# Optimization experiments

Measured on AMD Instinct MI355X. Metric: run time of the kernel, lower is better.

Reference implementation:

```python
import jax, jax.numpy as jnp
import numpy as np

B, S = 2, 2048          # 2 prompt sequences of 2048 tokens (packed: T = B*S)
H, KV, D, G = 32, 8, 128, 128   # heads, kv heads, head_dim, quant group size
THETA = 1e6


def _dequant(w_int, scales, g=G):
    # w_int: [O, I] int4 values in [-8, 7]; scales: [O, I//g] per-group fp scales
    return w_int.astype(jnp.float32) * jnp.repeat(scales, g, axis=1)


def _rope_neox(x, pos):
    # x: [B, S, h, D]; pos: [B, S]; neox style rotates (first half, second half)
    half = D // 2
    inv_freq = 1.0 / (THETA ** (jnp.arange(half, dtype=jnp.float32) / half))
    ang = pos[:, :, None] * inv_freq[None, None, :]          # [B, S, half]
    cos = jnp.cos(ang)[:, :, None, :]
    sin = jnp.sin(ang)[:, :, None, :]
    x1, x2 = x[..., :half], x[..., half:]
    return jnp.concatenate([x1 * cos - x2 * sin, x2 * cos + x1 * sin], axis=-1)


def setup_inputs() -> dict:
    key = jax.random.key(0)
    k1, k2, k3, k4, k5, k6 = jax.random.split(key, 6)
    T, HID = B * S, H * D
    q_hidden = jax.random.randint(k1, (T, HID), -127, 128, dtype=jnp.int32)  # int8 acts
    q_scale = jax.random.uniform(k2, (T,), dtype=jnp.float32) * 0.01 + 1e-4  # per-token scale
    q_sum = jnp.sum(q_hidden, axis=-1).astype(jnp.float32)                   # per-token int8 sum
    OUT_QKV = (H + 2 * KV) * D
    w_qkv = jax.random.randint(k3, (OUT_QKV, HID), -8, 8, dtype=jnp.int32)   # int4 weights
    s_qkv = jax.random.uniform(k4, (OUT_QKV, HID // G), dtype=jnp.float32) * 0.01 + 1e-4
    w_o = jax.random.randint(k5, (HID, HID), -8, 8, dtype=jnp.int32)
    s_o = jax.random.uniform(k6, (HID, HID // G), dtype=jnp.float32) * 0.01 + 1e-4
    return {"q_hidden": q_hidden, "q_scale": q_scale, "q_sum": q_sum,
            "w_qkv": w_qkv, "s_qkv": s_qkv, "w_o": w_o, "s_o": s_o}


def reference(q_hidden, q_scale, q_sum, w_qkv, s_qkv, w_o, s_o):
    T = q_hidden.shape[0]
    # W4A8 qkv_proj with dynamic per-token input scale (symmetric int4 -> sum unused)
    x = q_hidden.astype(jnp.float32) * q_scale[:, None]          # dequant activations
    qkv = x @ _dequant(w_qkv, s_qkv).T                            # [T, (H+2KV)*D]
    q_sz, kv_sz = H * D, KV * D
    q = qkv[:, :q_sz].reshape(B, S, H, D)
    k = qkv[:, q_sz:q_sz + kv_sz].reshape(B, S, KV, D)
    v = qkv[:, q_sz + kv_sz:].reshape(B, S, KV, D)
    # fused bias(none)+RoPE (neox, full head_dim)
    pos = jnp.broadcast_to(jnp.arange(S, dtype=jnp.float32), (B, S))
    q = _rope_neox(q, pos)
    k = _rope_neox(k, pos)
    # varlen causal flash attention (GQA: 4 q-heads per kv head)
    qg = q.reshape(B, S, KV, H // KV, D)
    scores = jnp.einsum('bsghd,btgd->bghst', qg, k) * (D ** -0.5)
    causal = jnp.tril(jnp.ones((S, S), dtype=bool))
    scores = jnp.where(causal[None, None, None], scores, -jnp.inf)
    p = jax.nn.softmax(scores, axis=-1)
    attn = jnp.einsum('bghst,btgd->bsghd', p, v).reshape(T, H * D)
    # invoke_quant_fuse_sum: per-token symmetric int8 requant of attn output
    amax = jnp.maximum(jnp.max(jnp.abs(attn), axis=-1, keepdims=True), 1e-6)
    a_scale = amax / 127.0
    attn_q = jnp.clip(jnp.round(attn / a_scale), -127.0, 127.0)
    # W4A8 o_proj
    out = (attn_q * a_scale) @ _dequant(w_o, s_o).T               # [T, H*D]
    return out
```

## Files before the change

### kernel.cpp

```cpp
#include <hip/hip_runtime.h>
#include <math.h>

#define B_ 2
#define S_ 2048
#define H_ 32
#define KV_ 8
#define D_ 128
#define T_ 4096
#define HID_ 4096
#define OQKV_ 6144

typedef __attribute__((ext_vector_type(4))) float f32x4;
typedef __attribute__((ext_vector_type(4))) int i32x4;
typedef __attribute__((ext_vector_type(8))) __bf16 bf16x8;
typedef __attribute__((ext_vector_type(8))) unsigned short u16x8;
typedef unsigned short u16;
typedef signed char s8;

__device__ __forceinline__ u16 f2b(float f) {
  unsigned x = __float_as_uint(f);
  return (u16)((x + 0x7FFFu + ((x >> 16) & 1u)) >> 16);
}
__device__ __forceinline__ float b2f(u16 u) {
  return __uint_as_float(((unsigned)u) << 16);
}

__device__ __forceinline__ void async16(const void* g, void* l) {
  __builtin_amdgcn_global_load_lds((__attribute__((address_space(1))) void*)g,
                                   (__attribute__((address_space(3))) void*)l,
                                   16, 0, 0);
}

__device__ __forceinline__ bf16x8 ld8(const u16* p) { return *(const bf16x8*)p; }

__device__ __forceinline__ f32x4 mfma16x16(bf16x8 a, bf16x8 b, f32x4 c) {
  return __builtin_amdgcn_mfma_f32_16x16x32_bf16(a, b, c, 0, 0, 0);
}

__device__ __forceinline__ bf16x8 ones8() {
  union { u16x8 u; bf16x8 b; } c;
  c.u = u16x8{0x3F80, 0x3F80, 0x3F80, 0x3F80, 0x3F80, 0x3F80, 0x3F80, 0x3F80};
  return c.b;
}

__global__ __launch_bounds__(256) void pack_i8(const int* __restrict__ w,
                                               s8* __restrict__ out) {
  size_t base = ((size_t)blockIdx.x * 256 + threadIdx.x) * 4;
  int4 v = *(const int4*)(w + base);
  unsigned r = (unsigned)(v.x & 255) | ((unsigned)(v.y & 255) << 8) |
               ((unsigned)(v.z & 255) << 16) | ((unsigned)v.w << 24);
  *(unsigned*)(out + base) = r;
}

__global__ __launch_bounds__(256) void rope_kernel(u16* __restrict__ qkv) {
  int idx = blockIdx.x * 256 + threadIdx.x;
  int t = idx / 2560;
  int r = idx - t * 2560;
  int head = r >> 6;
  int d = r & 63;
  int col = (head < 32) ? (head * 128 + d) : (4096 + (head - 32) * 128 + d);
  size_t base = (size_t)t * 6144 + col;
  float x1 = b2f(qkv[base]);
  float x2 = b2f(qkv[base + 64]);
  float e = (float)d * 0.015625f;
  float freq = exp2f(e * -19.931568569324174f);
  float ang = (float)(t & 2047) * freq;
  float sn, cs;
  sincosf(ang, &sn, &cs);
  qkv[base] = f2b(x1 * cs - x2 * sn);
  qkv[base + 64] = f2b(x2 * cs + x1 * sn);
}

__global__ __launch_bounds__(256) void vt_transpose(const u16* __restrict__ qkv,
                                                    u16* __restrict__ vt) {
  __shared__ u16 tile[64][65];
  const int s0 = blockIdx.x * 64, d0 = blockIdx.y * 64;
  const int bk = blockIdx.z, b = bk >> 3, kv = bk & 7;
  const int tid = threadIdx.x;
  const int rr = tid >> 3, cc = tid & 7;
#pragma unroll
  for (int it = 0; it < 2; it++) {
    int r = it * 32 + rr;
    u16x8 v = *(const u16x8*)(qkv + (size_t)(b * 2048 + s0 + r) * 6144 + 5120 +
                              kv * 128 + d0 + cc * 8);
#pragma unroll
    for (int k = 0; k < 8; k++) tile[r][cc * 8 + k] = v[k];
  }
  __syncthreads();
#pragma unroll
  for (int it = 0; it < 2; it++) {
    int d = it * 32 + rr;
    u16x8 o;
#pragma unroll
    for (int k = 0; k < 8; k++) o[k] = tile[cc * 8 + k][d];
    *(u16x8*)(vt + (size_t)(bk * 128 + d0 + d) * 2048 + s0 + cc * 8) = o;
  }
}

__device__ __forceinline__ void store_out(float* p, float v) { *p = v; }
__device__ __forceinline__ void store_out(u16* p, float v) { *p = f2b(v); }

template <typename OutT>
__global__ __launch_bounds__(256, 4) void gemm_i8(const s8* __restrict__ A,
                                                  const s8* __restrict__ Bw,
                                                  const float* __restrict__ sB,
                                                  const float* __restrict__ rowscale,
                                                  OutT* __restrict__ C,
                                                  int M, int N, int K) {
  __shared__ __align__(16) s8 As[128 * 128];
  __shared__ __align__(16) s8 Bs[64 * 128];
  __shared__ float Ss[64][33];
  const int tid = threadIdx.x;
  const int lane = tid & 63;
  const int wv = tid >> 6;
  const int m0 = blockIdx.y * 128, n0 = blockIdx.x * 64;
  const int g = lane >> 4, c15 = lane & 15;
  const int KG = K >> 7;

  for (int i = tid; i < 64 * 32; i += 256)
    Ss[i >> 5][i & 31] = sB[(size_t)n0 * 32 + i];

  f32x4 acc[2][4] = {};

  const int srow = lane >> 2;
  const int pch = lane & 3;
  const int scol = (((pch - (srow >> 1)) & 3)) * 16;
  const s8* Ag0 = A + (size_t)(m0 + (2 * wv) * 16 + srow) * K + scol;
  const s8* Ag1 = A + (size_t)(m0 + (2 * wv + 1) * 16 + srow) * K + scol;
  const s8* Bg = Bw + (size_t)(n0 + wv * 16 + srow) * K + scol;
  s8* Al0 = As + (2 * wv) * 1024 + lane * 16;
  s8* Al1 = As + (2 * wv + 1) * 1024 + lane * 16;
  s8* Bl = Bs + wv * 1024 + lane * 16;

  const int aoff = (wv * 32 + c15) * 64 + ((g + (c15 >> 1)) & 3) * 16;
  const int boff = c15 * 64 + ((g + (c15 >> 1)) & 3) * 16;

  for (int grp = 0; grp < KG; ++grp) {
    const int kb = grp << 7;
    __syncthreads();
    async16(Ag0 + kb, Al0);
    async16(Ag1 + kb, Al1);
    async16(Bg + kb, Bl);
    async16(Ag0 + kb + 64, Al0 + 8192);
    async16(Ag1 + kb + 64, Al1 + 8192);
    async16(Bg + kb + 64, Bl + 4096);
    __syncthreads();

    i32x4 iacc[2][4];
#pragma unroll
    for (int sub = 0; sub < 2; sub++) {
      i32x4 af[2], bf[4];
#pragma unroll
      for (int i = 0; i < 2; i++)
        af[i] = *(const i32x4*)(As + sub * 8192 + aoff + i * 1024);
#pragma unroll
      for (int j = 0; j < 4; j++)
        bf[j] = *(const i32x4*)(Bs + sub * 4096 + boff + j * 1024);
#pragma unroll
      for (int i = 0; i < 2; i++)
#pragma unroll
        for (int j = 0; j < 4; j++)
          iacc[i][j] = __builtin_amdgcn_mfma_i32_16x16x64_i8(
              af[i], bf[j], sub ? iacc[i][j] : (i32x4){0, 0, 0, 0}, 0, 0, 0);
    }
#pragma unroll
    for (int j = 0; j < 4; j++) {
      const float sc = Ss[j * 16 + c15][grp];
#pragma unroll
      for (int i = 0; i < 2; i++)
#pragma unroll
        for (int r = 0; r < 4; r++)
          acc[i][j][r] += sc * (float)iacc[i][j][r];
    }
  }

#pragma unroll
  for (int i = 0; i < 2; i++) {
#pragma unroll
    for (int r = 0; r < 4; r++) {
      int m = m0 + wv * 32 + i * 16 + g * 4 + r;
      float scm = rowscale[m];
#pragma unroll
      for (int j = 0; j < 4; j++) {
        int n = n0 + j * 16 + c15;
        store_out(C + (size_t)m * N + n, acc[i][j][r] * scm);
      }
    }
  }
}


struct AttnState {
  f32x4 acc[2][9];
  float mrun[2][4];
};

template <bool FULL>
__device__ __forceinline__ void qk_phase(int j0, int q0w, const u16* Ksp,
                                         const bf16x8 qf[2][4],
                                         f32x4 (&sc)[2][4], int g, int c15) {
  const int qmax = q0w + 31;
#pragma unroll
  for (int nt = 0; nt < 4; nt++) {
    if (FULL || (j0 + nt * 16 <= qmax)) {
      bf16x8 kf[4];
#pragma unroll
      for (int c = 0; c < 4; c++)
        kf[c] = ld8(Ksp + (nt * 16 + c15) * 128 +
                    (((g + 4 * c) ^ (c15 & 7)) * 8));
      f32x4 s0 = {0.f, 0.f, 0.f, 0.f}, s1 = {0.f, 0.f, 0.f, 0.f};
#pragma unroll
      for (int c = 0; c < 4; c++) {
        s0 = mfma16x16(qf[0][c], kf[c], s0);
        s1 = mfma16x16(qf[1][c], kf[c], s1);
      }
      if (FULL) {
#pragma unroll
        for (int r = 0; r < 4; r++) {
          sc[0][nt][r] = s0[r] * 0.08838834764831845f;
          sc[1][nt][r] = s1[r] * 0.08838834764831845f;
        }
      } else {
        const int key = j0 + nt * 16 + c15;
#pragma unroll
        for (int r = 0; r < 4; r++) {
          sc[0][nt][r] =
              (key <= q0w + g * 4 + r) ? s0[r] * 0.08838834764831845f : -INFINITY;
          sc[1][nt][r] =
              (key <= q0w + 16 + g * 4 + r) ? s1[r] * 0.08838834764831845f : -INFINITY;
        }
      }
    }
  }
}

template <bool FULL>
__device__ __forceinline__ void smax_pv(int j0, int q0w, const u16* Vsp,
                                        u16* pw0, u16* pw1, f32x4 (&sc)[2][4],
                                        AttnState& st, int g, int c15,
                                        const bf16x8 vones) {
  const int qmax = q0w + 31;
#pragma unroll
  for (int m = 0; m < 2; m++) {
    u16* pw = m ? pw1 : pw0;
    float alpha[4];
#pragma unroll
    for (int r = 0; r < 4; r++) {
      float rm = -INFINITY;
#pragma unroll
      for (int nt = 0; nt < 4; nt++)
        if (FULL || (j0 + nt * 16 <= qmax)) rm = fmaxf(rm, sc[m][nt][r]);
      rm = fmaxf(rm, __shfl_xor(rm, 1));
      rm = fmaxf(rm, __shfl_xor(rm, 2));
      rm = fmaxf(rm, __shfl_xor(rm, 4));
      rm = fmaxf(rm, __shfl_xor(rm, 8));
      float mnew = fmaxf(st.mrun[m][r], rm);
      alpha[r] = __expf(st.mrun[m][r] - mnew);
      st.mrun[m][r] = mnew;
#pragma unroll
      for (int nt = 0; nt < 4; nt++) {
        float pv = (FULL || (j0 + nt * 16 <= qmax))
                       ? __expf(sc[m][nt][r] - mnew) : 0.0f;
        pw[(g * 4 + r) * 72 + nt * 16 + c15] = f2b(pv);
      }
    }
#pragma unroll
    for (int dt = 0; dt < 9; dt++)
#pragma unroll
      for (int r = 0; r < 4; r++) st.acc[m][dt][r] *= alpha[r];
  }
#pragma unroll
  for (int kc = 0; kc < 2; kc++) {
    bf16x8 pf0 = ld8(pw0 + c15 * 72 + kc * 32 + g * 8);
    bf16x8 pf1 = ld8(pw1 + c15 * 72 + kc * 32 + g * 8);
#pragma unroll
    for (int dt = 0; dt < 8; dt++) {
      bf16x8 vf = ld8(Vsp + (dt * 16 + c15) * 64 +
                      (((g + 4 * kc) ^ (c15 & 7)) * 8));
      st.acc[0][dt] = mfma16x16(pf0, vf, st.acc[0][dt]);
      st.acc[1][dt] = mfma16x16(pf1, vf, st.acc[1][dt]);
    }
    st.acc[0][8] = mfma16x16(pf0, vones, st.acc[0][8]);
    st.acc[1][8] = mfma16x16(pf1, vones, st.acc[1][8]);
  }
}

__global__ __launch_bounds__(256, 2) void attn_kernel(const u16* __restrict__ qkvb,
                                                      const u16* __restrict__ vtb,
                                                      float* __restrict__ out) {
  __shared__ __align__(16) u16 Ks[64 * 128];
  __shared__ __align__(16) u16 Vs[2][128 * 64];
  __shared__ __align__(16) u16 Ps[4][2][16 * 72];
  const int tid = threadIdx.x, lane = tid & 63, wv = tid >> 6;
  const int g = lane >> 4, c15 = lane & 15;
  const int h = blockIdx.x, b = blockIdx.y, qb = 15 - (int)blockIdx.z;
  const int kvh = h >> 2;
  const int Q0 = qb * 128;
  const int q0w = Q0 + wv * 32;
  const int nsteps = 2 * qb + 2;
  const bf16x8 vones = ones8();
  u16* pw0 = &Ps[wv][0][0];
  u16* pw1 = &Ps[wv][1][0];

  const int keyl = lane >> 4, kch = lane & 15;
  const int dll = lane >> 3, vch = lane & 7;
  const u16* Kg = qkvb + (size_t)(b * 2048) * 6144 + 4096 + kvh * 128;
  const u16* Vg = vtb + (size_t)((b * 8 + kvh) * 128) * 2048;

  auto stageK = [&](int j0) {
#pragma unroll
    for (int i = 0; i < 4; i++) {
      const int key = wv * 16 + i * 4 + keyl;
      async16(Kg + (size_t)(j0 + key) * 6144 + ((kch ^ (key & 7)) * 8),
              (u16*)Ks + (wv * 16 + i * 4) * 128 + lane * 8);
    }
  };
  auto stageV = [&](int j0, int vb) {
#pragma unroll
    for (int i = 0; i < 4; i++) {
      const int d = wv * 32 + i * 8 + dll;
      async16(Vg + (size_t)d * 2048 + j0 + ((vch ^ (d & 7)) * 8),
              (u16*)&Vs[vb][0] + (wv * 32 + i * 8) * 64 + lane * 8);
    }
  };

  bf16x8 qf[2][4];
#pragma unroll
  for (int m = 0; m < 2; m++) {
    const u16* qp =
        qkvb + (size_t)(b * 2048 + q0w + m * 16 + c15) * 6144 + h * 128 + g * 8;
#pragma unroll
    for (int c = 0; c < 4; c++) qf[m][c] = ld8(qp + c * 32);
  }

  AttnState st;
#pragma unroll
  for (int m = 0; m < 2; m++) {
#pragma unroll
    for (int dt = 0; dt < 9; dt++) st.acc[m][dt] = f32x4{0.f, 0.f, 0.f, 0.f};
#pragma unroll
    for (int r = 0; r < 4; r++) st.mrun[m][r] = -INFINITY;
  }

  stageK(0);
  stageV(0, 0);

  for (int jt = 0; jt < nsteps; ++jt) {
    const int j0 = jt * 64;
    __syncthreads();
    const int mode = (j0 + 64 <= q0w) ? 0 : ((j0 <= q0w + 31) ? 1 : 2);
    f32x4 sc[2][4];
    if (mode == 0) qk_phase<true>(j0, q0w, (const u16*)Ks, qf, sc, g, c15);
    else if (mode == 1) qk_phase<false>(j0, q0w, (const u16*)Ks, qf, sc, g, c15);
    __syncthreads();
    if (jt + 1 < nsteps) {
      stageK(j0 + 64);
      stageV(j0 + 64, (jt + 1) & 1);
    }
    const u16* Vsp = (const u16*)&Vs[jt & 1][0];
    if (mode == 0) smax_pv<true>(j0, q0w, Vsp, pw0, pw1, sc, st, g, c15, vones);
    else if (mode == 1) smax_pv<false>(j0, q0w, Vsp, pw0, pw1, sc, st, g, c15, vones);
  }

#pragma unroll
  for (int m = 0; m < 2; m++)
#pragma unroll
    for (int r = 0; r < 4; r++) {
      const int row = q0w + m * 16 + g * 4 + r;
      float inv = 1.0f / st.acc[m][8][r];
      float* op = out + (size_t)(b * 2048 + row) * 4096 + h * 128;
#pragma unroll
      for (int dt = 0; dt < 8; dt++) op[dt * 16 + c15] = st.acc[m][dt][r] * inv;
    }
}

__global__ __launch_bounds__(256) void quant_kernel(const float* __restrict__ attn,
                                                    s8* __restrict__ aq,
                                                    float* __restrict__ ascale) {
  const int t = blockIdx.x, tid = threadIdx.x;
  const float* row = attn + (size_t)t * 4096;
  f32x4 v[4];
  float am = 0.f;
#pragma unroll
  for (int i = 0; i < 4; i++) {
    v[i] = *(const f32x4*)(row + tid * 16 + i * 4);
#pragma unroll
    for (int r = 0; r < 4; r++) am = fmaxf(am, fabsf(v[i][r]));
  }
#pragma unroll
  for (int m = 1; m <= 32; m <<= 1) am = fmaxf(am, __shfl_xor(am, m));
  __shared__ float red[4];
  if ((tid & 63) == 0) red[tid >> 6] = am;
  __syncthreads();
  am = fmaxf(fmaxf(red[0], red[1]), fmaxf(red[2], red[3]));
  float asc = fmaxf(am, 1e-6f) / 127.0f;
  if (tid == 0) ascale[t] = asc;
  int w[4];
#pragma unroll
  for (int i = 0; i < 4; i++) {
    int bytes[4];
#pragma unroll
    for (int r = 0; r < 4; r++) {
      float q = rintf(v[i][r] / asc);
      q = fminf(127.0f, fmaxf(-127.0f, q));
      bytes[r] = ((int)q) & 255;
    }
    w[i] = bytes[0] | (bytes[1] << 8) | (bytes[2] << 16) | (bytes[3] << 24);
  }
  *(int4*)(aq + (size_t)t * 4096 + tid * 16) = int4{w[0], w[1], w[2], w[3]};
}

extern "C" void kernel_launch(void* const* d_in, const int* in_sizes, int n_in,
                              void* d_out, int out_size, void* d_ws, size_t ws_size,
                              hipStream_t stream) {
  const int* q_hidden = (const int*)d_in[0];
  const float* q_scale = (const float*)d_in[1];
  const int* w_qkv = (const int*)d_in[3];
  const float* s_qkv = (const float*)d_in[4];
  const int* w_o = (const int*)d_in[5];
  const float* s_o = (const float*)d_in[6];
  float* out = (float*)d_out;

  char* ws = (char*)d_ws;
  const size_t MB = 1024 * 1024;
  s8* WB = (s8*)(ws);
  u16* QKVB = (u16*)(ws + 48 * MB);
  u16* VTB = (u16*)(ws);
  s8* ATTNQ = (s8*)(ws + 8 * MB);
  float* ASC = (float*)(ws + 25 * MB);
  s8* WOB = (s8*)(ws + 48 * MB);
  s8* XB = (s8*)d_out;

  pack_i8<<<16384, 256, 0, stream>>>(q_hidden, XB);
  pack_i8<<<24576, 256, 0, stream>>>(w_qkv, WB);
  gemm_i8<u16><<<dim3(96, 32), 256, 0, stream>>>(XB, WB, s_qkv, q_scale, QKVB,
                                                 T_, OQKV_, HID_);
  rope_kernel<<<40960, 256, 0, stream>>>(QKVB);
  vt_transpose<<<dim3(32, 2, 16), 256, 0, stream>>>(QKVB, VTB);
  attn_kernel<<<dim3(32, 2, 16), 256, 0, stream>>>(QKVB, VTB, out);
  quant_kernel<<<4096, 256, 0, stream>>>(out, ATTNQ, ASC);
  pack_i8<<<16384, 256, 0, stream>>>(w_o, WOB);
  gemm_i8<float><<<dim3(64, 32), 256, 0, stream>>>(ATTNQ, WOB, s_o, ASC, out,
                                                   T_, HID_, HID_);
}
```

Baseline: 665.1 us.

## Double-buffer int8 GEMM K-tiles with async LDS loads and manual waitcnt

The W4A8 int8 GEMM used to load a full 128-wide K slab and sync twice per group, so global loads and MFMA never overlapped. It now keeps two 64-wide LDS buffers and issues the next half-tile's global_load_lds while the current one is consumed. Raw s_barrier and s_waitcnt vmcnt replace __syncthreads, and the loop is software-pipelined across the two halves. Shared memory use stays the same. Correctness now depends on the hand-written vmcnt counts matching the compiler's ordering of memory operations.

Result: slower. 719.1 us (+8.1%).

```diff
diff --git a/kernel.cpp b/kernel.cpp
--- a/kernel.cpp
+++ b/kernel.cpp
@@ -42,6 +42,9 @@
   c.u = u16x8{0x3F80, 0x3F80, 0x3F80, 0x3F80, 0x3F80, 0x3F80, 0x3F80, 0x3F80};
   return c.b;
 }
+
+#define SBAR() asm volatile("s_barrier" ::: "memory")
+#define WAITV(n) asm volatile("s_waitcnt vmcnt(" #n ")" ::: "memory")
 
 __global__ __launch_bounds__(256) void pack_i8(const int* __restrict__ w,
                                                s8* __restrict__ out) {
@@ -107,8 +110,8 @@
                                                   const float* __restrict__ rowscale,
                                                   OutT* __restrict__ C,
                                                   int M, int N, int K) {
-  __shared__ __align__(16) s8 As[128 * 128];
-  __shared__ __align__(16) s8 Bs[64 * 128];
+  __shared__ __align__(16) s8 As[2][128 * 64];
+  __shared__ __align__(16) s8 Bs[2][64 * 64];
   __shared__ float Ss[64][33];
   const int tid = threadIdx.x;
   const int lane = tid & 63;
@@ -116,6 +119,7 @@
   const int m0 = blockIdx.y * 128, n0 = blockIdx.x * 64;
   const int g = lane >> 4, c15 = lane & 15;
   const int KG = K >> 7;
+  const int NT = K >> 6;
 
   for (int i = tid; i < 64 * 32; i += 256)
     Ss[i >> 5][i & 31] = sB[(size_t)n0 * 32 + i];
@@ -128,40 +132,77 @@
   const s8* Ag0 = A + (size_t)(m0 + (2 * wv) * 16 + srow) * K + scol;
   const s8* Ag1 = A + (size_t)(m0 + (2 * wv + 1) * 16 + srow) * K + scol;
   const s8* Bg = Bw + (size_t)(n0 + wv * 16 + srow) * K + scol;
-  s8* Al0 = As + (2 * wv) * 1024 + lane * 16;
-  s8* Al1 = As + (2 * wv + 1) * 1024 + lane * 16;
-  s8* Bl = Bs + wv * 1024 + lane * 16;
+  const int la0 = (2 * wv) * 1024 + lane * 16;
+  const int la1 = (2 * wv + 1) * 1024 + lane * 16;
+  const int lb = wv * 1024 + lane * 16;
 
   const int aoff = (wv * 32 + c15) * 64 + ((g + (c15 >> 1)) & 3) * 16;
   const int boff = c15 * 64 + ((g + (c15 >> 1)) & 3) * 16;
 
+  async16(Ag0, &As[0][0] + la0);
+  async16(Ag1, &As[0][0] + la1);
+  async16(Bg, &Bs[0][0] + lb);
+  async16(Ag0 + 64, &As[1][0] + la0);
+  async16(Ag1 + 64, &As[1][0] + la1);
+  async16(Bg + 64, &Bs[1][0] + lb);
+  asm volatile("s_waitcnt vmcnt(3) lgkmcnt(0)" ::: "memory");
+  SBAR();
+
   for (int grp = 0; grp < KG; ++grp) {
-    const int kb = grp << 7;
-    __syncthreads();
-    async16(Ag0 + kb, Al0);
-    async16(Ag1 + kb, Al1);
-    async16(Bg + kb, Bl);
-    async16(Ag0 + kb + 64, Al0 + 8192);
-    async16(Ag1 + kb + 64, Al1 + 8192);
-    async16(Bg + kb + 64, Bl + 4096);
-    __syncthreads();
-
     i32x4 iacc[2][4];
-#pragma unroll
-    for (int sub = 0; sub < 2; sub++) {
+    {
       i32x4 af[2], bf[4];
 #pragma unroll
       for (int i = 0; i < 2; i++)
-        af[i] = *(const i32x4*)(As + sub * 8192 + aoff + i * 1024);
+        af[i] = *(const i32x4*)(&As[0][0] + aoff + i * 1024);
 #pragma unroll
       for (int j = 0; j < 4; j++)
-        bf[j] = *(const i32x4*)(Bs + sub * 4096 + boff + j * 1024);
+        bf[j] = *(const i32x4*)(&Bs[0][0] + boff + j * 1024);
 #pragma unroll
       for (int i = 0; i < 2; i++)
 #pragma unroll
         for (int j = 0; j < 4; j++)
           iacc[i][j] = __builtin_amdgcn_mfma_i32_16x16x64_i8(
-              af[i], bf[j], sub ? iacc[i][j] : (i32x4){0, 0, 0, 0}, 0, 0, 0);
+              af[i], bf[j], (i32x4){0, 0, 0, 0}, 0, 0, 0);
+    }
+    SBAR();
+    {
+      const int t2 = 2 * grp + 2;
+      if (t2 < NT) {
+        const int kb = t2 << 6;
+        async16(Ag0 + kb, &As[0][0] + la0);
+        async16(Ag1 + kb, &As[0][0] + la1);
+        async16(Bg + kb, &Bs[0][0] + lb);
+        WAITV(3);
+      } else {
+        WAITV(0);
+      }
+    }
+    SBAR();
+    {
+      i32x4 af[2], bf[4];
+#pragma unroll
+      for (int i = 0; i < 2; i++)
+        af[i] = *(const i32x4*)(&As[1][0] + aoff + i * 1024);
+#pragma unroll
+      for (int j = 0; j < 4; j++)
+        bf[j] = *(const i32x4*)(&Bs[1][0] + boff + j * 1024);
+#pragma unroll
+      for (int i = 0; i < 2; i++)
+#pragma unroll
+        for (int j = 0; j < 4; j++)
+          iacc[i][j] = __builtin_amdgcn_mfma_i32_16x16x64_i8(
+              af[i], bf[j], iacc[i][j], 0, 0, 0);
+    }
+    SBAR();
+    {
+      const int t3 = 2 * grp + 3;
+      if (t3 < NT) {
+        const int kb = t3 << 6;
+        async16(Ag0 + kb, &As[1][0] + la0);
+        async16(Ag1 + kb, &As[1][0] + la1);
+        async16(Bg + kb, &Bs[1][0] + lb);
+      }
     }
 #pragma unroll
     for (int j = 0; j < 4; j++) {
@@ -172,6 +213,8 @@
         for (int r = 0; r < 4; r++)
           acc[i][j][r] += sc * (float)iacc[i][j][r];
     }
+    if (2 * grp + 3 < NT) { WAITV(3); } else { WAITV(0); }
+    SBAR();
   }
 
 #pragma unroll
@@ -188,7 +231,6 @@
     }
   }
 }
-
 
 struct AttnState {
   f32x4 acc[2][9];
```
